# Optimization experiments

Measured on AMD Instinct MI355X. Metric: run time of the kernel, lower is better.

## Reference

```python
import jax, jax.numpy as jnp
import numpy as np

INPUT_SIZE = (224, 224)


def setup_inputs() -> dict:
    key = jax.random.key(0)
    k1, k2, k3 = jax.random.split(key, 3)
    feat2 = jax.random.normal(k1, (16, 512, 28, 28), dtype=jnp.float32)
    feat3 = jax.random.normal(k2, (16, 1024, 14, 14), dtype=jnp.float32)
    memory_bank = jax.random.normal(k3, (16384, 1536), dtype=jnp.float32)
    return {"feat2": feat2, "feat3": feat3, "memory_bank": memory_bank}


def reference(feat2, feat3, memory_bank):
    b, c2, h, w = feat2.shape
    c3 = feat3.shape[1]
    # interpolate(feat3, size=(h,w), mode='bilinear', align_corners=False)
    feat3_up = jax.image.resize(feat3, (b, c3, h, w), method='bilinear')
    features = jnp.concatenate([feat2, feat3_up], axis=1)  # [b, c, h, w]
    c = c2 + c3
    feats = features.transpose(0, 2, 3, 1).reshape(-1, c)  # [N, c]
    x_sq = jnp.sum(feats * feats, axis=1, keepdims=True)            # [N, 1]
    m_sq = jnp.sum(memory_bank * memory_bank, axis=1)[None, :]      # [1, M]
    d2 = x_sq + m_sq - 2.0 * (feats @ memory_bank.T)                # [N, M]
    min_d = jnp.sqrt(jnp.maximum(jnp.min(d2, axis=1), 0.0))         # [N]
    anomaly_map = min_d.reshape(b, 1, h, w)
    anomaly_map = jax.image.resize(
        anomaly_map, (b, 1, INPUT_SIZE[0], INPUT_SIZE[1]), method='bilinear')
    pred_score = jnp.max(anomaly_map.reshape(b, -1), axis=1)
    return anomaly_map, pred_score
```

## Files before the change

### kernel.cpp

```cpp
#include <hip/hip_runtime.h>
#include <math.h>

#define N_ROWS 12544
#define C_DIM  1536
#define M_ROWS 16384
#define BATCH  16

#define QS    16.0f
#define S2x2  0.0078125f
#define S2    0.00390625f

typedef int   i32x4 __attribute__((ext_vector_type(4)));
typedef unsigned char u8;
typedef signed char   i8;

__device__ __forceinline__ unsigned fkey(float f) {
  unsigned u = __float_as_uint(f);
  return (u & 0x80000000u) ? ~u : (u | 0x80000000u);
}
__device__ __forceinline__ float funkey(unsigned k) {
  unsigned u = (k & 0x80000000u) ? (k ^ 0x80000000u) : ~k;
  return __uint_as_float(u);
}

__device__ __forceinline__ void gl_lds16(const void* g, void* l) {
  __builtin_amdgcn_global_load_lds(
      (__attribute__((address_space(1))) void*)(g),
      (__attribute__((address_space(3))) void*)(l), 16, 0, 0);
}

__device__ __forceinline__ int quant(float v) {
  int q = __float2int_rn(v * QS);
  return max(-127, min(127, q));
}

#define FSTRIDE 528

__global__ __launch_bounds__(512) void prep_all(
    const float* __restrict__ feat2, const float* __restrict__ feat3,
    const float* __restrict__ mb,
    i8* __restrict__ feats, i8* __restrict__ mbb,
    int* __restrict__ xsqp, float* __restrict__ msq,
    unsigned* __restrict__ dmin, unsigned* __restrict__ score) {
  const int blk = blockIdx.x;
  const int t = threadIdx.x;
  __shared__ u8 fsm[28 * FSTRIDE];
  __shared__ int sxq[28];

  if (blk >= 1344) {
    const int wave = t >> 6, lane = t & 63;
    const int row = (blk - 1344) * 8 + wave;
    const float* in = mb + (size_t)row * C_DIM;
    i8* outp = mbb + (size_t)row * C_DIM;
    float ssq = 0.f;
#pragma unroll
    for (int i = 0; i < 6; i++) {
      const int f4 = lane + 64 * i;
      const float4 v = *(const float4*)(in + f4 * 4);
      int q0 = quant(v.x), q1 = quant(v.y), q2 = quant(v.z), q3 = quant(v.w);
      unsigned w = (unsigned)(q0 & 0xFF) | ((unsigned)(q1 & 0xFF) << 8)
                 | ((unsigned)(q2 & 0xFF) << 16) | ((unsigned)(q3 & 0xFF) << 24);
      *(unsigned*)(outp + f4 * 4) = w;
      ssq += (float)(q0*q0 + q1*q1 + q2*q2 + q3*q3);
    }
    for (int off = 32; off > 0; off >>= 1) ssq += __shfl_down(ssq, off, 64);
    if (lane == 0) msq[row] = S2 * ssq;
  } else {
    const int half = blk % 3, p = blk / 3;
    const int b = p / 28, y = p % 28;
    const int n0 = b * 784 + y * 28;

    const float sy = 0.5f * y - 0.25f;
    const int y0 = (int)floorf(sy); const float fy = sy - (float)y0;
    const int y0c = max(y0, 0), y1c = min(y0 + 1, 13);
    const float wy0 = 1.f - fy, wy1 = fy;

    const int g  = t >> 5;
    const int l2 = t & 31;
    const float sx = 0.5f * l2 - 0.25f;
    const int x0 = (int)floorf(sx); const float fx = sx - (float)x0;
    const int x0c = max(x0, 0), x1c = min(x0 + 1, 13);
    const float wx0 = 1.f - fx, wx1 = fx;

    if (t < 28) sxq[t] = 0;

    if (half == 0) {
      const float* f2b = feat2 + (size_t)b * 512 * 784 + y * 28;
#pragma unroll 4
      for (int i = 0; i < 32; i++) {
        const int c = i * 16 + g;
        if (l2 < 28) {
          float v = f2b[(size_t)c * 784 + l2];
          fsm[l2 * FSTRIDE + c] = (u8)(i8)quant(v);
        }
      }
    } else {
      const int cc0 = (half - 1) * 512;
      const float* f3b = feat3 + (size_t)b * 1024 * 196;
#pragma unroll 4
      for (int i = 0; i < 32; i++) {
        const int cc = cc0 + i * 16 + g;
        const float* f3 = f3b + (size_t)cc * 196;
        float v = 0.f;
        if (l2 < 14)       v = f3[y0c * 14 + l2];
        else if (l2 < 28)  v = f3[y1c * 14 + (l2 - 14)];
        float t0 = wy0 * __shfl(v, x0c, 32)     + wy1 * __shfl(v, 14 + x0c, 32);
        float t1 = wy0 * __shfl(v, x1c, 32)     + wy1 * __shfl(v, 14 + x1c, 32);
        if (l2 < 28) {
          float o = wx0 * t0 + wx1 * t1;
          fsm[l2 * FSTRIDE + (i * 16 + g)] = (u8)(i8)quant(o);
        }
      }
    }
    __syncthreads();

    const int c0 = half * 512;
    i8* orow = feats + (size_t)n0 * C_DIM + c0;
    for (int idx = t; idx < 28 * 32; idx += 512) {
      const int row = idx / 32, col = idx % 32;
      i32x4 wv = *(const i32x4*)(fsm + row * FSTRIDE + col * 16);
      *(i32x4*)(orow + (size_t)row * C_DIM + col * 16) = wv;
      int s = 0;
#pragma unroll
      for (int k = 0; k < 4; k++) {
        const int w = wv[k];
        const int b0 = (int)(i8)(w & 0xFF), b1 = (int)(i8)((w >> 8) & 0xFF);
        const int b2 = (int)(i8)((w >> 16) & 0xFF), b3 = (int)(i8)(w >> 24);
        s += b0*b0 + b1*b1 + b2*b2 + b3*b3;
      }
      atomicAdd(&sxq[row], s);
    }
    __syncthreads();
    if (t < 28) {
      xsqp[half * N_ROWS + n0 + t] = sxq[t];
      if (half == 0) dmin[n0 + t] = 0xFFFFFFFFu;
    }
    if (blk == 0 && t < BATCH) score[t] = 0u;
  }
}

__global__ __launch_bounds__(256) void gemm_min(
    const i8* __restrict__ X, const i8* __restrict__ Mb,
    const float* __restrict__ msq, unsigned* __restrict__ dmin) {
  __shared__ u8 As[16384];
  __shared__ u8 Bs[16384];
  __shared__ unsigned smin[128];
  const int t = threadIdx.x;
  const int bx = blockIdx.x;
  const int mtile = ((bx & 7) << 4) | (bx >> 3);
  const int ntile = blockIdx.y;
  const int lane = t & 63, wave = t >> 6;
  const int wm = wave >> 1, wn = wave & 1;
  if (t < 128) smin[t] = 0xFFFFFFFFu;

  const int row0 = ntile * 128;
  const int col0 = mtile * 128;
  const int s_row = t >> 2;
  const int s_ch  = (t & 3) ^ ((t >> 3) & 3);
  const i8* ga = X  + (size_t)(row0 + s_row) * C_DIM + s_ch * 16;
  const i8* gb = Mb + (size_t)(col0 + s_row) * C_DIM + s_ch * 16;
  u8* la = As + t * 16;
  u8* lb = Bs + t * 16;

  i32x4 acc[4][4];
  const i32x4 zero = {0, 0, 0, 0};
#pragma unroll
  for (int mi = 0; mi < 4; mi++)
#pragma unroll
    for (int ni = 0; ni < 4; ni++) acc[mi][ni] = zero;

  const int quad = lane >> 4, l16 = lane & 15;
  const int fsw = (l16 >> 1) & 3;
  const int slot = ((quad ^ fsw) * 16);
  const u8* arow = As + (wm * 64 + l16) * 64 + slot;
  const u8* brow = Bs + (wn * 64 + l16) * 64 + slot;

#define STAGE(BUF, KS) { \
    gl_lds16(ga + (KS) * 64,                 la + (BUF) * 8192); \
    gl_lds16(ga + 64 * C_DIM + (KS) * 64,    la + (BUF) * 8192 + 4096); \
    gl_lds16(gb + (KS) * 64,                 lb + (BUF) * 8192); \
    gl_lds16(gb + 64 * C_DIM + (KS) * 64,    lb + (BUF) * 8192 + 4096); }
#define COMPUTE(BUF) { \
    i32x4 af[4], bf[4]; \
    _Pragma("unroll") \
    for (int mi = 0; mi < 4; mi++) \
      af[mi] = *(const i32x4*)(arow + (BUF) * 8192 + mi * 1024); \
    _Pragma("unroll") \
    for (int ni = 0; ni < 4; ni++) \
      bf[ni] = *(const i32x4*)(brow + (BUF) * 8192 + ni * 1024); \
    _Pragma("unroll") \
    for (int mi = 0; mi < 4; mi++) \
      _Pragma("unroll") \
      for (int ni = 0; ni < 4; ni++) \
        acc[mi][ni] = __builtin_amdgcn_mfma_i32_16x16x64_i8( \
            af[mi], bf[ni], acc[mi][ni], 0, 0, 0); }
#define VM4  asm volatile("s_waitcnt vmcnt(4)" ::: "memory")
#define VM0  asm volatile("s_waitcnt vmcnt(0)" ::: "memory")
#define BARR asm volatile("s_barrier" ::: "memory")

  STAGE(0, 0);
  for (int ks = 0; ks < 22; ks += 2) {
    STAGE(1, ks + 1);
    VM4; BARR;
    COMPUTE(0);
    BARR;
    STAGE(0, ks + 2);
    VM4; BARR;
    COMPUTE(1);
    BARR;
  }
  STAGE(1, 23);
  VM4; BARR;
  COMPUTE(0);
  BARR;
  VM0; BARR;
  COMPUTE(1);

#undef BARR
#undef VM0
#undef VM4
#undef COMPUTE
#undef STAGE

  float msql[4];
#pragma unroll
  for (int ni = 0; ni < 4; ni++)
    msql[ni] = msq[col0 + wn * 64 + ni * 16 + l16];

#pragma unroll
  for (int mi = 0; mi < 4; mi++) {
#pragma unroll
    for (int r = 0; r < 4; r++) {
      float v = msql[0] - S2x2 * (float)acc[mi][0][r];
#pragma unroll
      for (int ni = 1; ni < 4; ni++)
        v = fminf(v, msql[ni] - S2x2 * (float)acc[mi][ni][r]);
      v = fminf(v, __shfl_xor(v, 1, 64));
      v = fminf(v, __shfl_xor(v, 2, 64));
      v = fminf(v, __shfl_xor(v, 4, 64));
      v = fminf(v, __shfl_xor(v, 8, 64));
      if (l16 == 0) {
        int lrow = wm * 64 + mi * 16 + quad * 4 + r;
        atomicMin(&smin[lrow], fkey(v));
      }
    }
  }
  __syncthreads();
  if (t < 128) atomicMin(&dmin[row0 + t], smin[t]);
}

__global__ void finalize(const unsigned* __restrict__ dmin,
                         const int* __restrict__ xsqp,
                         float* __restrict__ out) {
  const int b = blockIdx.x, slice = blockIdx.y, t = threadIdx.x;
  __shared__ float smap[784];
  __shared__ float sred[4];
  for (int i = t; i < 784; i += 256) {
    const int idx = b * 784 + i;
    const int xs = xsqp[idx] + xsqp[N_ROWS + idx] + xsqp[2 * N_ROWS + idx];
    float d2 = S2 * (float)xs + funkey(dmin[idx]);
    smap[i] = sqrtf(fmaxf(d2, 0.f));
  }
  __syncthreads();
  float* omap = out + (size_t)b * 50176;
  float tmax = 0.f;
  const int p0 = slice * 6272;
  for (int p = p0 + t; p < p0 + 6272; p += 256) {
    const int Y = p / 224, Xp = p % 224;
    const float sy = Y * 0.125f - 0.4375f;
    const float sx = Xp * 0.125f - 0.4375f;
    const int y0 = (int)floorf(sy); const float fy = sy - (float)y0;
    const int x0 = (int)floorf(sx); const float fx = sx - (float)x0;
    const int y0c = max(y0, 0), y1c = min(y0 + 1, 27);
    const int x0c = max(x0, 0), x1c = min(x0 + 1, 27);
    float v = (1.f-fy)*((1.f-fx)*smap[y0c*28+x0c] + fx*smap[y0c*28+x1c])
            +      fy *((1.f-fx)*smap[y1c*28+x0c] + fx*smap[y1c*28+x1c]);
    omap[p] = v;
    tmax = fmaxf(tmax, v);
  }
  for (int off = 32; off > 0; off >>= 1)
    tmax = fmaxf(tmax, __shfl_down(tmax, off, 64));
  if ((t & 63) == 0) sred[t >> 6] = tmax;
  __syncthreads();
  if (t == 0) {
    float m = fmaxf(fmaxf(sred[0], sred[1]), fmaxf(sred[2], sred[3]));
    atomicMax((unsigned*)(out + 802816 + b), __float_as_uint(m));
  }
}

extern "C" void kernel_launch(void* const* d_in, const int* in_sizes, int n_in,
                              void* d_out, int out_size, void* d_ws, size_t ws_size,
                              hipStream_t stream) {
  const float* feat2 = (const float*)d_in[0];
  const float* feat3 = (const float*)d_in[1];
  const float* mb    = (const float*)d_in[2];
  char* ws = (char*)d_ws;
  i8*       feats = (i8*)ws;
  i8*       mbb   = (i8*)(ws + 19267584);
  int*      xsqp  = (int*)(ws + 44433408);
  float*    msq   = (float*)(ws + 44583936);
  unsigned* dmin  = (unsigned*)(ws + 44649472);
  float* out = (float*)d_out;

  prep_all<<<1344 + 2048, 512, 0, stream>>>(
      feat2, feat3, mb, feats, mbb, xsqp, msq, dmin,
      (unsigned*)(out + 802816));
  gemm_min<<<dim3(128, 98), 256, 0, stream>>>(feats, mbb, msq, dmin);
  finalize<<<dim3(BATCH, 8), 256, 0, stream>>>(dmin, xsqp, out);
}
```

Baseline: 564.0 us.

## Streamline GEMM double-buffer barriers and replace LDS atomics with wave shuffle reduction

The int8 GEMM main loop drops the manual vmcnt waits and the two s_barriers per stage. It now issues the next stage's global-to-LDS loads, computes on the current buffer, and relies on one __syncthreads per half-iteration, with the K offset advanced by pointer increments. In the feature-prep kernel, per-row squared-norm accumulation moves from shared-memory atomics to a 32-lane shuffle reduction with a single write per row, which makes the zero-init of that shared array unnecessary. The prep loops are also unrolled further. The GEMM change trades explicit fine-grained wait control for fewer barriers and relies on __syncthreads also waiting on the outstanding loads.

Result: no change. 572.0 us (+1.4%).

```diff
diff --git a/kernel.cpp b/kernel.cpp
--- a/kernel.cpp
+++ b/kernel.cpp
@@ -82,11 +82,9 @@
     const int x0c = max(x0, 0), x1c = min(x0 + 1, 13);
     const float wx0 = 1.f - fx, wx1 = fx;
 
-    if (t < 28) sxq[t] = 0;
-
     if (half == 0) {
       const float* f2b = feat2 + (size_t)b * 512 * 784 + y * 28;
-#pragma unroll 4
+#pragma unroll 8
       for (int i = 0; i < 32; i++) {
         const int c = i * 16 + g;
         if (l2 < 28) {
@@ -97,7 +95,7 @@
     } else {
       const int cc0 = (half - 1) * 512;
       const float* f3b = feat3 + (size_t)b * 1024 * 196;
-#pragma unroll 4
+#pragma unroll 8
       for (int i = 0; i < 32; i++) {
         const int cc = cc0 + i * 16 + g;
         const float* f3 = f3b + (size_t)cc * 196;
@@ -116,19 +114,28 @@
 
     const int c0 = half * 512;
     i8* orow = feats + (size_t)n0 * C_DIM + c0;
-    for (int idx = t; idx < 28 * 32; idx += 512) {
-      const int row = idx / 32, col = idx % 32;
-      i32x4 wv = *(const i32x4*)(fsm + row * FSTRIDE + col * 16);
-      *(i32x4*)(orow + (size_t)row * C_DIM + col * 16) = wv;
-      int s = 0;
-#pragma unroll
-      for (int k = 0; k < 4; k++) {
-        const int w = wv[k];
-        const int b0 = (int)(i8)(w & 0xFF), b1 = (int)(i8)((w >> 8) & 0xFF);
-        const int b2 = (int)(i8)((w >> 16) & 0xFF), b3 = (int)(i8)(w >> 24);
-        s += b0*b0 + b1*b1 + b2*b2 + b3*b3;
+#pragma unroll
+    for (int pass = 0; pass < 2; ++pass) {
+      const int idx = t + pass * 512;
+      if (idx < 896) {
+        const int row = idx >> 5, col = idx & 31;
+        i32x4 wv = *(const i32x4*)(fsm + row * FSTRIDE + col * 16);
+        *(i32x4*)(orow + (size_t)row * C_DIM + col * 16) = wv;
+        int s = 0;
+#pragma unroll
+        for (int k = 0; k < 4; k++) {
+          const int w = wv[k];
+          const int b0 = (int)(i8)(w & 0xFF), b1 = (int)(i8)((w >> 8) & 0xFF);
+          const int b2 = (int)(i8)((w >> 16) & 0xFF), b3 = (int)(i8)(w >> 24);
+          s += b0*b0 + b1*b1 + b2*b2 + b3*b3;
+        }
+        s += __shfl_xor(s, 1, 32);
+        s += __shfl_xor(s, 2, 32);
+        s += __shfl_xor(s, 4, 32);
+        s += __shfl_xor(s, 8, 32);
+        s += __shfl_xor(s, 16, 32);
+        if (col == 0) sxq[row] = s;
       }
-      atomicAdd(&sxq[row], s);
     }
     __syncthreads();
     if (t < 28) {
@@ -175,11 +182,11 @@
   const u8* arow = As + (wm * 64 + l16) * 64 + slot;
   const u8* brow = Bs + (wn * 64 + l16) * 64 + slot;
 
-#define STAGE(BUF, KS) { \
-    gl_lds16(ga + (KS) * 64,                 la + (BUF) * 8192); \
-    gl_lds16(ga + 64 * C_DIM + (KS) * 64,    la + (BUF) * 8192 + 4096); \
-    gl_lds16(gb + (KS) * 64,                 lb + (BUF) * 8192); \
-    gl_lds16(gb + 64 * C_DIM + (KS) * 64,    lb + (BUF) * 8192 + 4096); }
+#define STAGE(BUF, KOFF) { \
+    gl_lds16(ga + (KOFF),                 la + (BUF) * 8192); \
+    gl_lds16(ga + 64 * C_DIM + (KOFF),    la + (BUF) * 8192 + 4096); \
+    gl_lds16(gb + (KOFF),                 lb + (BUF) * 8192); \
+    gl_lds16(gb + 64 * C_DIM + (KOFF),    lb + (BUF) * 8192 + 4096); }
 #define COMPUTE(BUF) { \
     i32x4 af[4], bf[4]; \
     _Pragma("unroll") \
@@ -194,31 +201,23 @@
       for (int ni = 0; ni < 4; ni++) \
         acc[mi][ni] = __builtin_amdgcn_mfma_i32_16x16x64_i8( \
             af[mi], bf[ni], acc[mi][ni], 0, 0, 0); }
-#define VM4  asm volatile("s_waitcnt vmcnt(4)" ::: "memory")
-#define VM0  asm volatile("s_waitcnt vmcnt(0)" ::: "memory")
-#define BARR asm volatile("s_barrier" ::: "memory")
 
   STAGE(0, 0);
-  for (int ks = 0; ks < 22; ks += 2) {
-    STAGE(1, ks + 1);
-    VM4; BARR;
+  __syncthreads();
+  for (int it = 0; it < 11; ++it) {
+    STAGE(1, 64);
     COMPUTE(0);
-    BARR;
-    STAGE(0, ks + 2);
-    VM4; BARR;
+    __syncthreads();
+    ga += 128; gb += 128;
+    STAGE(0, 0);
     COMPUTE(1);
-    BARR;
-  }
-  STAGE(1, 23);
-  VM4; BARR;
+    __syncthreads();
+  }
+  STAGE(1, 64);
   COMPUTE(0);
-  BARR;
-  VM0; BARR;
+  __syncthreads();
   COMPUTE(1);
 
-#undef BARR
-#undef VM0
-#undef VM4
 #undef COMPUTE
 #undef STAGE
 
```
